# Kernel tuning notes

Hardware: AMD Instinct MI355X
Metric: run time of the kernel (lower is better)

Reference implementation:

```python
import jax, jax.numpy as jnp
import numpy as np

NUM_CLASSES = 2
IGNORE_INDEX = 0
B, H, W = 4, 512, 512
BIG_I = 2 ** 30  # int sentinel for 'no seed yet'
INF = jnp.float32(1e9)  # distance when a column/image has no seed


def _edt_to_seed(seed):
    """Exact 2D Euclidean distance transform: distance from every pixel to the
    nearest True pixel in `seed` [H, W] (matches scipy distance_transform_edt
    applied to an image whose zeros are `seed`).
    Pass 1: 1D nearest-seed distance down each column via cummax/cummin scans.
    Pass 2: exact lower envelope across rows by brute-force min over k:
            D^2(i,j) = min_k ( (j-k)^2 + g(i,k)^2 ).
    """
    h, w = seed.shape
    rows = jnp.arange(h, dtype=jnp.int32)[:, None]              # [H,1]
    last = jax.lax.cummax(jnp.where(seed, rows, -1), axis=0)     # last seed above
    d_fwd = jnp.where(last >= 0, rows - last, BIG_I)
    nxt = jax.lax.cummin(jnp.where(seed, rows, BIG_I), axis=0, reverse=True)
    d_bwd = jnp.where(nxt < BIG_I, nxt - rows, BIG_I)
    g = jnp.minimum(d_fwd, d_bwd)                                # [H,W] int
    g2 = jnp.where(g >= BIG_I // 2, INF * INF, (g * g).astype(jnp.float32))
    cols = jnp.arange(w, dtype=jnp.float32)
    sq = (cols[:, None] - cols[None, :]) ** 2                    # [Wj,Wk]
    d2 = jnp.min(g2[:, None, :] + sq[None, :, :], axis=-1)       # [H,Wj]
    return jnp.sqrt(d2)


def _distance_map_one(tgt):
    """tgt: [H, W] int labels -> [num_classes, H, W] signed distance maps."""
    maps = []
    for c in range(NUM_CLASSES):
        if c == IGNORE_INDEX:
            maps.append(jnp.zeros(tgt.shape, jnp.float32))
            continue
        mask = tgt == c
        pos_dist = _edt_to_seed(~mask)   # edt(posmask): dist to nearest background
        neg_dist = _edt_to_seed(mask)    # edt(negmask): dist to nearest foreground
        present = jnp.any(mask)          # 'if mask.sum() > 0' guard
        maps.append(jnp.where(present, neg_dist - pos_dist, 0.0))
    return jnp.stack(maps, axis=0)


def setup_inputs() -> dict:
    key = jax.random.key(0)
    k1, k2 = jax.random.split(key)
    pred = jax.random.normal(k1, (B, NUM_CLASSES, H, W), dtype=jnp.float32)
    target = jax.random.randint(k2, (B, H, W), 0, 2, dtype=jnp.int32)
    return {"pred": pred, "target": target}


def reference(pred, target):
    p = jax.nn.softmax(pred, axis=1)                         # [B,C,H,W]
    # sequential over batch to bound the [H,W,W] EDT intermediate
    dmaps = jax.lax.map(_distance_map_one, target)           # [B,C,H,W]
    return jnp.mean(p * dmaps)
```

## Files before the change

### kernel.cpp

```cpp
#include <hip/hip_runtime.h>
#include <math.h>

#define BB 4
#define HH 512
#define WW 512
#define HWSZ (HH * WW)

#define TCOLS 16
#define TCH   16
#define CROWS 32


__global__ __launch_bounds__(256) void edt_cols_kernel(
    const int* __restrict__ target,
    unsigned int* __restrict__ gpack,
    int* __restrict__ counts)
{
    int blk = blockIdx.x;
    int b = blk >> 5;
    int tile = blk & 31;
    int tid = threadIdx.x;
    int c = tid & (TCOLS - 1);
    int ch = tid >> 4;
    int j = tile * TCOLS + c;
    int r0 = ch * CROWS;

    const int* t = target + b * HWSZ + j;

    unsigned int maskN = 0;
#pragma unroll
    for (int i = 0; i < CROWS; ++i)
        maskN |= (unsigned int)(t[(r0 + i) * WW] == 1) << i;
    unsigned int maskP = ~maskN;

    __shared__ short sLastN[TCH][TCOLS], sLastP[TCH][TCOLS];
    __shared__ short sFirstN[TCH][TCOLS], sFirstP[TCH][TCOLS];
    __shared__ short sBefN[TCH][TCOLS], sBefP[TCH][TCOLS];
    __shared__ short sAftN[TCH][TCOLS], sAftP[TCH][TCOLS];
    __shared__ int sCnt;

    sLastN[ch][c]  = maskN ? (short)(r0 + 31 - __builtin_clz(maskN)) : (short)-1;
    sFirstN[ch][c] = maskN ? (short)(r0 + __builtin_ctz(maskN))      : (short)-1;
    sLastP[ch][c]  = maskP ? (short)(r0 + 31 - __builtin_clz(maskP)) : (short)-1;
    sFirstP[ch][c] = maskP ? (short)(r0 + __builtin_ctz(maskP))      : (short)-1;
    if (tid == 0) sCnt = 0;
    __syncthreads();

    if (tid < TCOLS) {
        short befN = -1, befP = -1;
        for (int k = 0; k < TCH; ++k) {
            sBefN[k][tid] = befN; sBefP[k][tid] = befP;
            short ln = sLastN[k][tid], lp = sLastP[k][tid];
            if (ln >= 0) befN = ln;
            if (lp >= 0) befP = lp;
        }
        short aftN = -1, aftP = -1;
        for (int k = TCH - 1; k >= 0; --k) {
            sAftN[k][tid] = aftN; sAftP[k][tid] = aftP;
            short fn = sFirstN[k][tid], fp = sFirstP[k][tid];
            if (fn >= 0) aftN = fn;
            if (fp >= 0) aftP = fp;
        }
    }
    atomicAdd(&sCnt, __popc(maskN));
    __syncthreads();

    int befN = sBefN[ch][c], befP = sBefP[ch][c];
    int aftN = sAftN[ch][c], aftP = sAftP[ch][c];
    unsigned int* gp = gpack + b * HWSZ + j;

#pragma unroll
    for (int i = 0; i < CROWS; ++i) {
        int row = r0 + i;
        unsigned int belowN = maskN << (31 - i);
        unsigned int aboveN = maskN >> i;
        unsigned int dfN = belowN ? (unsigned int)__builtin_clz(belowN)
                                  : (befN >= 0 ? (unsigned int)(row - befN) : 0xFFFFu);
        unsigned int dbN = aboveN ? (unsigned int)__builtin_ctz(aboveN)
                                  : (aftN >= 0 ? (unsigned int)(aftN - row) : 0xFFFFu);
        unsigned int gN = dfN < dbN ? dfN : dbN;

        unsigned int belowP = maskP << (31 - i);
        unsigned int aboveP = maskP >> i;
        unsigned int dfP = belowP ? (unsigned int)__builtin_clz(belowP)
                                  : (befP >= 0 ? (unsigned int)(row - befP) : 0xFFFFu);
        unsigned int dbP = aboveP ? (unsigned int)__builtin_ctz(aboveP)
                                  : (aftP >= 0 ? (unsigned int)(aftP - row) : 0xFFFFu);
        unsigned int gP = dfP < dbP ? dfP : dbP;

        gp[row * WW] = gN | (gP << 16);
    }

    if (tid == 0) counts[blk] = sCnt;
}

__global__ __launch_bounds__(256) void edt_rows_kernel(
    const unsigned int* __restrict__ gpack,
    const float* __restrict__ pred,
    double* __restrict__ partials)
{
    __shared__ float g2n[WW];
    __shared__ float g2p[WW];
    __shared__ double red[256];

    int bi = blockIdx.x;
    int b = bi >> 9;
    int i = bi & (HH - 1);
    int tid = threadIdx.x;

    const unsigned int* gp = gpack + b * HWSZ + i * WW;
    for (int k = tid; k < WW; k += 256) {
        unsigned int pk = gp[k];
        unsigned int gN = pk & 0xFFFFu;
        unsigned int gP = pk >> 16;
        g2n[k] = (gN == 0xFFFFu) ? 1e18f : (float)(gN * gN);
        g2p[k] = (gP == 0xFFFFu) ? 1e18f : (float)(gP * gP);
    }
    __syncthreads();

    const float* p0 = pred + (b * 2 + 0) * HWSZ + i * WW;
    const float* p1 = pred + (b * 2 + 1) * HWSZ + i * WW;

    double local = 0.0;
    for (int j = tid; j < WW; j += 256) {
        float bn = g2n[j];
        float bp = g2p[j];
        for (int r = 1; r < WW; ++r) {
            float sq = (float)(r * r);
            if (sq >= bn && sq >= bp) break;
            int kl = j - r;
            int kr = j + r;
            if (kl >= 0) {
                bn = fminf(bn, sq + g2n[kl]);
                bp = fminf(bp, sq + g2p[kl]);
            }
            if (kr < WW) {
                bn = fminf(bn, sq + g2n[kr]);
                bp = fminf(bp, sq + g2p[kr]);
            }
        }
        float dist = sqrtf(bn) - sqrtf(bp);
        float prob = 1.0f / (1.0f + expf(p0[j] - p1[j]));
        local += (double)(prob * dist);
    }

    red[tid] = local;
    __syncthreads();
    for (int off = 128; off > 0; off >>= 1) {
        if (tid < off) red[tid] += red[tid + off];
        __syncthreads();
    }
    if (tid == 0) partials[bi] = red[0];
}

__global__ __launch_bounds__(256) void finalize_kernel(
    const int* __restrict__ counts,
    const double* __restrict__ partials,
    float* __restrict__ out)
{
    __shared__ int sPres[BB];
    __shared__ double red[256];
    int tid = threadIdx.x;

    if (tid < BB) sPres[tid] = 0;
    __syncthreads();
    if (tid < 128) atomicAdd(&sPres[tid >> 5], counts[tid]);
    __syncthreads();

    double s = 0.0;
    for (int idx = tid; idx < BB * HH; idx += 256) {
        double g = (sPres[idx >> 9] > 0) ? 1.0 : 0.0;
        s += partials[idx] * g;
    }
    red[tid] = s;
    __syncthreads();
    for (int off = 128; off > 0; off >>= 1) {
        if (tid < off) red[tid] += red[tid + off];
        __syncthreads();
    }
    if (tid == 0)
        out[0] = (float)(red[0] * (1.0 / 2097152.0));
}

extern "C" void kernel_launch(void* const* d_in, const int* in_sizes, int n_in,
                              void* d_out, int out_size, void* d_ws, size_t ws_size,
                              hipStream_t stream) {
    const float* pred = (const float*)d_in[0];
    const int* target = (const int*)d_in[1];
    float* out = (float*)d_out;

    char* ws = (char*)d_ws;
    int* counts = (int*)(ws + 0);
    double* partials = (double*)(ws + 1024);
    unsigned int* gpack = (unsigned int*)(ws + 32768);

    edt_cols_kernel<<<BB * (WW / TCOLS), 256, 0, stream>>>(target, gpack, counts);
    edt_rows_kernel<<<BB * HH, 256, 0, stream>>>(gpack, pred, partials);
    finalize_kernel<<<1, 256, 0, stream>>>(counts, partials, out);
}
```

Baseline: 76.02 us.

## Rework EDT column scan with wave shuffles and row pass with one wave per row

The column kernel moves to 512 threads with 16-row chunks and replaces the serial per-column before/after scan with wave shuffle prefix max/min scans; the popcount uses a wave reduction. The row kernel now runs one 64-thread wave per row, each lane owning 8 contiguous columns with a shared early-exit test. It uses padded shared arrays to avoid bank conflicts, vectorized pred loads and a shuffle reduction in place of the shared-memory tree. The common break condition for all 8 columns may do extra iterations compared with per-column exits, and accumulation is now float per lane.

```diff
diff --git a/kernel.cpp b/kernel.cpp
--- a/kernel.cpp
+++ b/kernel.cpp
@@ -7,11 +7,14 @@
 #define HWSZ (HH * WW)
 
 #define TCOLS 16
-#define TCH   16
-#define CROWS 32
-
-
-__global__ __launch_bounds__(256) void edt_cols_kernel(
+#define TCH   32
+#define CROWS 16
+#define COLS_BLOCKS (BB * (WW / TCOLS))
+#define ROWS_BLOCKS (BB * HH)
+#define BIGR 0x100000
+
+
+__global__ __launch_bounds__(512) void edt_cols_kernel(
     const int* __restrict__ target,
     unsigned int* __restrict__ gpack,
     int* __restrict__ counts)
@@ -31,42 +34,53 @@
 #pragma unroll
     for (int i = 0; i < CROWS; ++i)
         maskN |= (unsigned int)(t[(r0 + i) * WW] == 1) << i;
-    unsigned int maskP = ~maskN;
-
-    __shared__ short sLastN[TCH][TCOLS], sLastP[TCH][TCOLS];
-    __shared__ short sFirstN[TCH][TCOLS], sFirstP[TCH][TCOLS];
-    __shared__ short sBefN[TCH][TCOLS], sBefP[TCH][TCOLS];
-    __shared__ short sAftN[TCH][TCOLS], sAftP[TCH][TCOLS];
+    unsigned int maskP = maskN ^ 0xFFFFu;
+
+    __shared__ int sLN[TCH][TCOLS], sFN[TCH][TCOLS];
+    __shared__ int sLP[TCH][TCOLS], sFP[TCH][TCOLS];
+    __shared__ int sBN[TCH][TCOLS], sAN[TCH][TCOLS];
+    __shared__ int sBP[TCH][TCOLS], sAP[TCH][TCOLS];
     __shared__ int sCnt;
 
-    sLastN[ch][c]  = maskN ? (short)(r0 + 31 - __builtin_clz(maskN)) : (short)-1;
-    sFirstN[ch][c] = maskN ? (short)(r0 + __builtin_ctz(maskN))      : (short)-1;
-    sLastP[ch][c]  = maskP ? (short)(r0 + 31 - __builtin_clz(maskP)) : (short)-1;
-    sFirstP[ch][c] = maskP ? (short)(r0 + __builtin_ctz(maskP))      : (short)-1;
+    sLN[ch][c] = maskN ? (r0 + 31 - __builtin_clz(maskN)) : -1;
+    sFN[ch][c] = maskN ? (r0 + __builtin_ctz(maskN))      : BIGR;
+    sLP[ch][c] = maskP ? (r0 + 31 - __builtin_clz(maskP)) : -1;
+    sFP[ch][c] = maskP ? (r0 + __builtin_ctz(maskP))      : BIGR;
+
+    int cnt = __popc(maskN);
+#pragma unroll
+    for (int off = 32; off > 0; off >>= 1) cnt += __shfl_down(cnt, off, 64);
     if (tid == 0) sCnt = 0;
     __syncthreads();
-
-    if (tid < TCOLS) {
-        short befN = -1, befP = -1;
-        for (int k = 0; k < TCH; ++k) {
-            sBefN[k][tid] = befN; sBefP[k][tid] = befP;
-            short ln = sLastN[k][tid], lp = sLastP[k][tid];
-            if (ln >= 0) befN = ln;
-            if (lp >= 0) befP = lp;
-        }
-        short aftN = -1, aftP = -1;
-        for (int k = TCH - 1; k >= 0; --k) {
-            sAftN[k][tid] = aftN; sAftP[k][tid] = aftP;
-            short fn = sFirstN[k][tid], fp = sFirstP[k][tid];
-            if (fn >= 0) aftN = fn;
-            if (fp >= 0) aftP = fp;
-        }
-    }
-    atomicAdd(&sCnt, __popc(maskN));
-    __syncthreads();
-
-    int befN = sBefN[ch][c], befP = sBefP[ch][c];
-    int aftN = sAftN[ch][c], aftP = sAftP[ch][c];
+    if ((tid & 63) == 0) atomicAdd(&sCnt, cnt);
+
+    int w = tid >> 6, lane = tid & 63;
+    int cc = 2 * w + (lane >> 5);
+    int c2 = lane & 31;
+    int iLN = sLN[c2][cc], iLP = sLP[c2][cc];
+    int iFN = sFN[c2][cc], iFP = sFP[c2][cc];
+#pragma unroll
+    for (int d = 1; d < 32; d <<= 1) {
+        int uLN = __shfl_up(iLN, d, 64);
+        int uLP = __shfl_up(iLP, d, 64);
+        if (c2 >= d) { iLN = max(iLN, uLN); iLP = max(iLP, uLP); }
+    }
+#pragma unroll
+    for (int d = 1; d < 32; d <<= 1) {
+        int dFN = __shfl_down(iFN, d, 64);
+        int dFP = __shfl_down(iFP, d, 64);
+        if (c2 + d < 32) { iFN = min(iFN, dFN); iFP = min(iFP, dFP); }
+    }
+    int bLN = __shfl_up(iLN, 1, 64);  if (c2 == 0)  bLN = -1;
+    int bLP = __shfl_up(iLP, 1, 64);  if (c2 == 0)  bLP = -1;
+    int aFN = __shfl_down(iFN, 1, 64); if (c2 == 31) aFN = BIGR;
+    int aFP = __shfl_down(iFP, 1, 64); if (c2 == 31) aFP = BIGR;
+    sBN[c2][cc] = bLN; sBP[c2][cc] = bLP;
+    sAN[c2][cc] = aFN; sAP[c2][cc] = aFP;
+    __syncthreads();
+
+    int befN = sBN[ch][c], befP = sBP[ch][c];
+    int aftN = sAN[ch][c], aftP = sAP[ch][c];
     unsigned int* gp = gpack + b * HWSZ + j;
 
 #pragma unroll
@@ -77,16 +91,18 @@
         unsigned int dfN = belowN ? (unsigned int)__builtin_clz(belowN)
                                   : (befN >= 0 ? (unsigned int)(row - befN) : 0xFFFFu);
         unsigned int dbN = aboveN ? (unsigned int)__builtin_ctz(aboveN)
-                                  : (aftN >= 0 ? (unsigned int)(aftN - row) : 0xFFFFu);
+                                  : (aftN < BIGR ? (unsigned int)(aftN - row) : 0xFFFFu);
         unsigned int gN = dfN < dbN ? dfN : dbN;
+        if (gN > 0xFFFFu) gN = 0xFFFFu;
 
         unsigned int belowP = maskP << (31 - i);
         unsigned int aboveP = maskP >> i;
         unsigned int dfP = belowP ? (unsigned int)__builtin_clz(belowP)
                                   : (befP >= 0 ? (unsigned int)(row - befP) : 0xFFFFu);
         unsigned int dbP = aboveP ? (unsigned int)__builtin_ctz(aboveP)
-                                  : (aftP >= 0 ? (unsigned int)(aftP - row) : 0xFFFFu);
+                                  : (aftP < BIGR ? (unsigned int)(aftP - row) : 0xFFFFu);
         unsigned int gP = dfP < dbP ? dfP : dbP;
+        if (gP > 0xFFFFu) gP = 0xFFFFu;
 
         gp[row * WW] = gN | (gP << 16);
     }
@@ -94,63 +110,79 @@
     if (tid == 0) counts[blk] = sCnt;
 }
 
-__global__ __launch_bounds__(256) void edt_rows_kernel(
+#define SK(x) ((x) + ((x) >> 5))
+
+__global__ __launch_bounds__(64) void edt_rows_kernel(
     const unsigned int* __restrict__ gpack,
     const float* __restrict__ pred,
     double* __restrict__ partials)
 {
-    __shared__ float g2n[WW];
-    __shared__ float g2p[WW];
-    __shared__ double red[256];
+    __shared__ float g2n[SK(511) + 1];
+    __shared__ float g2p[SK(511) + 1];
 
     int bi = blockIdx.x;
     int b = bi >> 9;
     int i = bi & (HH - 1);
-    int tid = threadIdx.x;
+    int k = threadIdx.x;
+    int j0 = 8 * k;
+
+    const float* p0 = pred + (b * 2 + 0) * HWSZ + i * WW + j0;
+    const float* p1 = pred + (b * 2 + 1) * HWSZ + i * WW + j0;
+    float4 a0 = *(const float4*)(p0);
+    float4 a1 = *(const float4*)(p0 + 4);
+    float4 c0 = *(const float4*)(p1);
+    float4 c1 = *(const float4*)(p1 + 4);
 
     const unsigned int* gp = gpack + b * HWSZ + i * WW;
-    for (int k = tid; k < WW; k += 256) {
-        unsigned int pk = gp[k];
-        unsigned int gN = pk & 0xFFFFu;
-        unsigned int gP = pk >> 16;
-        g2n[k] = (gN == 0xFFFFu) ? 1e18f : (float)(gN * gN);
-        g2p[k] = (gP == 0xFFFFu) ? 1e18f : (float)(gP * gP);
-    }
-    __syncthreads();
-
-    const float* p0 = pred + (b * 2 + 0) * HWSZ + i * WW;
-    const float* p1 = pred + (b * 2 + 1) * HWSZ + i * WW;
-
-    double local = 0.0;
-    for (int j = tid; j < WW; j += 256) {
-        float bn = g2n[j];
-        float bp = g2p[j];
-        for (int r = 1; r < WW; ++r) {
-            float sq = (float)(r * r);
-            if (sq >= bn && sq >= bp) break;
-            int kl = j - r;
-            int kr = j + r;
-            if (kl >= 0) {
-                bn = fminf(bn, sq + g2n[kl]);
-                bp = fminf(bp, sq + g2p[kl]);
-            }
-            if (kr < WW) {
-                bn = fminf(bn, sq + g2n[kr]);
-                bp = fminf(bp, sq + g2p[kr]);
-            }
+    unsigned int pk[8];
+#pragma unroll
+    for (int t = 0; t < 8; ++t) pk[t] = gp[k + 64 * t];
+#pragma unroll
+    for (int t = 0; t < 8; ++t) {
+        int idx = k + 64 * t;
+        unsigned int gN = pk[t] & 0xFFFFu;
+        unsigned int gP = pk[t] >> 16;
+        g2n[SK(idx)] = (gN == 0xFFFFu) ? 1e18f : (float)(gN * gN);
+        g2p[SK(idx)] = (gP == 0xFFFFu) ? 1e18f : (float)(gP * gP);
+    }
+    __syncthreads();
+
+    float bn[8], bp[8];
+#pragma unroll
+    for (int jj = 0; jj < 8; ++jj) {
+        bn[jj] = g2n[SK(j0 + jj)];
+        bp[jj] = g2p[SK(j0 + jj)];
+    }
+    for (int r = 1; r < WW; ++r) {
+        float sq = (float)(r * r);
+        float mx = 0.0f;
+#pragma unroll
+        for (int jj = 0; jj < 8; ++jj) mx = fmaxf(mx, fmaxf(bn[jj], bp[jj]));
+        if (sq >= mx) break;
+#pragma unroll
+        for (int jj = 0; jj < 8; ++jj) {
+            int kl = j0 + jj - r; kl = kl < 0 ? 0 : kl;
+            int kr = j0 + jj + r; kr = kr > (WW - 1) ? (WW - 1) : kr;
+            int skl = SK(kl), skr = SK(kr);
+            bn[jj] = fminf(bn[jj], sq + g2n[skl]);
+            bp[jj] = fminf(bp[jj], sq + g2p[skl]);
+            bn[jj] = fminf(bn[jj], sq + g2n[skr]);
+            bp[jj] = fminf(bp[jj], sq + g2p[skr]);
         }
-        float dist = sqrtf(bn) - sqrtf(bp);
-        float prob = 1.0f / (1.0f + expf(p0[j] - p1[j]));
-        local += (double)(prob * dist);
-    }
-
-    red[tid] = local;
-    __syncthreads();
-    for (int off = 128; off > 0; off >>= 1) {
-        if (tid < off) red[tid] += red[tid + off];
-        __syncthreads();
-    }
-    if (tid == 0) partials[bi] = red[0];
+    }
+
+    float x0[8] = {a0.x, a0.y, a0.z, a0.w, a1.x, a1.y, a1.z, a1.w};
+    float x1[8] = {c0.x, c0.y, c0.z, c0.w, c1.x, c1.y, c1.z, c1.w};
+    float acc = 0.0f;
+#pragma unroll
+    for (int jj = 0; jj < 8; ++jj) {
+        float dist = sqrtf(bn[jj]) - sqrtf(bp[jj]);
+        float prob = 1.0f / (1.0f + __expf(x0[jj] - x1[jj]));
+        acc += prob * dist;
+    }
+#pragma unroll
+    for (int off = 32; off > 0; off >>= 1) acc += __shfl_down(acc, off, 64);
+    if (k == 0) partials[bi] = (double)acc;
 }
 
 __global__ __launch_bounds__(256) void finalize_kernel(
@@ -158,20 +190,19 @@
     const double* __restrict__ partials,
     float* __restrict__ out)
 {
-    __shared__ int sPres[BB];
     __shared__ double red[256];
+    __shared__ int pres[BB];
     int tid = threadIdx.x;
 
-    if (tid < BB) sPres[tid] = 0;
-    __syncthreads();
-    if (tid < 128) atomicAdd(&sPres[tid >> 5], counts[tid]);
+    if (tid < BB) pres[tid] = 0;
+    __syncthreads();
+    if (tid < COLS_BLOCKS && counts[tid] > 0)
+        atomicOr(&pres[tid >> 5], 1);
     __syncthreads();
 
     double s = 0.0;
-    for (int idx = tid; idx < BB * HH; idx += 256) {
-        double g = (sPres[idx >> 9] > 0) ? 1.0 : 0.0;
-        s += partials[idx] * g;
-    }
+    for (int idx = tid; idx < ROWS_BLOCKS; idx += 256)
+        s += pres[idx >> 9] ? partials[idx] : 0.0;
     red[tid] = s;
     __syncthreads();
     for (int off = 128; off > 0; off >>= 1) {
@@ -194,7 +225,7 @@
     double* partials = (double*)(ws + 1024);
     unsigned int* gpack = (unsigned int*)(ws + 32768);
 
-    edt_cols_kernel<<<BB * (WW / TCOLS), 256, 0, stream>>>(target, gpack, counts);
-    edt_rows_kernel<<<BB * HH, 256, 0, stream>>>(gpack, pred, partials);
+    edt_cols_kernel<<<COLS_BLOCKS, 512, 0, stream>>>(target, gpack, counts);
+    edt_rows_kernel<<<ROWS_BLOCKS, 64, 0, stream>>>(gpack, pred, partials);
     finalize_kernel<<<1, 256, 0, stream>>>(counts, partials, out);
 }
```

After: 75.12 us. About the same (-1.2%).
